# Kernel tuning notes

Measured on AMD Instinct MI355X. Metric: run time of the kernel, lower is better.

The kernel has to match this reference:

```python
import jax, jax.numpy as jnp
import numpy as np

D = 1024

def setup_inputs() -> dict:
    key = jax.random.key(0)
    k1, k2, k3, k4, k5 = jax.random.split(key, 5)
    B, S = 128, 512
    seq_output = jax.random.normal(k1, (B, S, D), dtype=jnp.float32)
    mask = jax.random.randint(k2, (B, S), 0, 2) == 1  # True = masked position
    # ensure last position is never fully-masked pathological: fine either way
    scale1 = 1.0 / np.sqrt(D)
    W1 = jax.random.normal(k3, (D, D), dtype=jnp.float32) * scale1
    b1 = jnp.zeros((D,), dtype=jnp.float32)
    w2 = jax.random.normal(k4, (D,), dtype=jnp.float32) * scale1
    return {"seq_output": seq_output, "mask": mask, "W1": W1, "b1": b1, "w2": w2}

def reference(seq_output, mask, W1, b1, w2):
    # u_last: last timestep embedding
    u_last = seq_output[:, -1, :]                           # [B, D]
    # additive attention MLP: Linear -> tanh -> Linear(D->1, no bias)
    h = jnp.tanh(jnp.einsum('bsd,de->bse', seq_output, W1) + b1)  # [B, S, D]
    scores = jnp.einsum('bsd,d->bs', h, w2)                 # [B, S]
    scores = jnp.where(mask, -1e9, scores)
    attn = jax.nn.softmax(scores, axis=-1)                  # [B, S]
    u_att = jnp.einsum('bs,bsd->bd', attn, seq_output)      # [B, D]
    return (u_last, u_att)
```

## Files before the change

### kernel.cpp

```cpp
#include <hip/hip_runtime.h>
#include <hip/hip_bf16.h>
#include <cstdint>
#include <cstddef>

#define BATCH 128
#define SEQ   512
#define DIM   1024
#define MROWS (BATCH * SEQ)
#define NT    32

typedef short short8 __attribute__((ext_vector_type(8)));
typedef __bf16 bf16x8 __attribute__((ext_vector_type(8)));
typedef float f32x4 __attribute__((ext_vector_type(4)));

template <typename VA> struct other_frag { using type = bf16x8; };
template <> struct other_frag<bf16x8> { using type = short8; };

template <typename VA>
__device__ __forceinline__ auto try_mfma(VA a, VA b, f32x4 c, int)
    -> decltype(__builtin_amdgcn_mfma_f32_16x16x32_bf16(a, b, c, 0, 0, 0)) {
  return __builtin_amdgcn_mfma_f32_16x16x32_bf16(a, b, c, 0, 0, 0);
}
template <typename VA>
__device__ __forceinline__ f32x4 try_mfma(VA a, VA b, f32x4 c, long) {
  using O = typename other_frag<VA>::type;
  O a2 = __builtin_bit_cast(O, a);
  O b2 = __builtin_bit_cast(O, b);
  return __builtin_amdgcn_mfma_f32_16x16x32_bf16(a2, b2, c, 0, 0, 0);
}
__device__ __forceinline__ f32x4 mfma_bf16(short8 a, short8 b, f32x4 c) {
  return try_mfma(a, b, c, 0);
}

__device__ __forceinline__ unsigned short f32_to_bf16(float f) {
  union { float f; uint32_t u; } v; v.f = f;
  uint32_t u = v.u;
  u += 0x7FFFu + ((u >> 16) & 1u);
  return (unsigned short)(u >> 16);
}

__device__ __forceinline__ short8 cvt8(f32x4 a, f32x4 b) {
  bf16x8 o;
  o[0] = (__bf16)a[0]; o[1] = (__bf16)a[1]; o[2] = (__bf16)a[2]; o[3] = (__bf16)a[3];
  o[4] = (__bf16)b[0]; o[5] = (__bf16)b[1]; o[6] = (__bf16)b[2]; o[7] = (__bf16)b[3];
  return __builtin_bit_cast(short8, o);
}

__device__ __forceinline__ void gload_lds16(const void* g, void* l) {
  __builtin_amdgcn_global_load_lds(
      (__attribute__((address_space(1))) void*)g,
      (__attribute__((address_space(3))) void*)l,
      16, 0, 0);
}

__device__ __forceinline__ float fast_tanh(float x) {
  x = fminf(fmaxf(x, -15.0f), 15.0f);
  float e = __expf(2.0f * x);
  return (e - 1.0f) / (e + 1.0f);
}

__global__ __launch_bounds__(256) void w1t_kernel(const float* __restrict__ W1,
                                                  unsigned short* __restrict__ W1t) {
  __shared__ float tile[64][65];
  int bx = blockIdx.x & 15;
  int by = blockIdx.x >> 4;
  int t = threadIdx.x;
  int c = t & 63, r0 = t >> 6;
#pragma unroll
  for (int i = 0; i < 16; i++) {
    int r = i * 4 + r0;
    tile[r][c] = W1[(size_t)(by * 64 + r) * DIM + bx * 64 + c];
  }
  __syncthreads();
#pragma unroll
  for (int i = 0; i < 16; i++) {
    int r = i * 4 + r0;
    W1t[(size_t)(bx * 64 + r) * DIM + by * 64 + c] = f32_to_bf16(tile[c][r]);
  }
}

__global__ __launch_bounds__(512, 2) void gemm_score_kernel(
    const float* __restrict__ X,
    const unsigned short* __restrict__ W1t,
    const float* __restrict__ b1,
    const float* __restrict__ w2,
    float* __restrict__ scores) {
  __shared__ __align__(16) char lds[147456];

  const int tid = threadIdx.x;
  const int lane = tid & 63;
  const int w = tid >> 6;
  const int wr = w >> 1, wc = w & 1;

  const int bx = blockIdx.x;
  const int swz = (bx & 7) * 128 + (bx >> 3);
  const int m0 = (swz >> 2) * 256;
  const int n0 = (swz & 3) * 256;

  const float* aSrc[4];
#pragma unroll
  for (int i = 0; i < 4; i++) {
    int sc = i * 512 + tid;
    int row = sc >> 3;
    int q = (sc & 7) ^ (row & 7) ^ ((row >> 3) & 7);
    aSrc[i] = X + (size_t)(m0 + row) * DIM + q * 4;
  }
  const unsigned short* bSrc[2];
#pragma unroll
  for (int i = 0; i < 2; i++) {
    int sc = i * 512 + tid;
    int srow = sc >> 3;
    int j = (sc & 7) ^ (srow & 7);
    int row = srow * 2 + (j >> 2);
    bSrc[i] = W1t + (size_t)(n0 + row) * DIM + (j & 3) * 8;
  }

  int aOff[4][2];
#pragma unroll
  for (int mi = 0; mi < 4; mi++) {
    int row = wr * 64 + mi * 16 + (lane & 15);
    int m = (row & 7) ^ ((row >> 3) & 7);
#pragma unroll
    for (int c = 0; c < 2; c++) {
      int js = ((lane >> 4) * 2 + c) ^ m;
      aOff[mi][c] = row * 128 + js * 16;
    }
  }
  int bOff[8];
#pragma unroll
  for (int ni = 0; ni < 8; ni++) {
    int row = wc * 128 + ni * 16 + (lane & 15);
    int srow = row >> 1;
    int ic = ((row & 1) * 4 + (lane >> 4)) ^ (srow & 7);
    bOff[ni] = srow * 128 + ic * 16;
  }

  f32x4 acc[4][8];
#pragma unroll
  for (int mi = 0; mi < 4; mi++)
#pragma unroll
    for (int ni = 0; ni < 8; ni++)
      acc[mi][ni] = (f32x4){0.f, 0.f, 0.f, 0.f};

  short8 af[4], bfv[8];

#define STAGE(S) do {                                                   \
    const int bufA_ = ((S) % 3) * 32768;                                \
    const int bufB_ = 98304 + ((S) % 3) * 16384;                        \
    const int koF_ = (S) * 32;                                          \
    gload_lds16(aSrc[0] + koF_, lds + bufA_ + w * 1024);                \
    gload_lds16(aSrc[1] + koF_, lds + bufA_ + 8192 + w * 1024);         \
    gload_lds16(aSrc[2] + koF_, lds + bufA_ + 16384 + w * 1024);        \
    gload_lds16(aSrc[3] + koF_, lds + bufA_ + 24576 + w * 1024);        \
    gload_lds16(bSrc[0] + koF_, lds + bufB_ + w * 1024);                \
    gload_lds16(bSrc[1] + koF_, lds + bufB_ + 8192 + w * 1024);         \
  } while (0)

#define KITER(S, VMSTR) do {                                            \
    asm volatile("s_waitcnt vmcnt(" VMSTR ")" ::: "memory");            \
    __builtin_amdgcn_s_barrier();                                       \
    __builtin_amdgcn_sched_barrier(0);                                  \
    if ((S) + 2 < NT) STAGE((S) + 2);                                   \
    const char* bufA_ = lds + ((S) % 3) * 32768;                        \
    const char* bufB_ = lds + 98304 + ((S) % 3) * 16384;                \
    _Pragma("unroll")                                                   \
    for (int mi = 0; mi < 4; mi++) {                                    \
      f32x4 lo_ = *(const f32x4*)(bufA_ + aOff[mi][0]);                 \
      f32x4 hi_ = *(const f32x4*)(bufA_ + aOff[mi][1]);                 \
      af[mi] = cvt8(lo_, hi_);                                          \
    }                                                                   \
    _Pragma("unroll")                                                   \
    for (int ni = 0; ni < 8; ni++)                                      \
      bfv[ni] = *(const short8*)(bufB_ + bOff[ni]);                     \
    __builtin_amdgcn_s_setprio(1);                                      \
    _Pragma("unroll")                                                   \
    for (int mi = 0; mi < 4; mi++)                                      \
      _Pragma("unroll")                                                 \
      for (int ni = 0; ni < 8; ni++)                                    \
        acc[mi][ni] = mfma_bf16(af[mi], bfv[ni], acc[mi][ni]);          \
    __builtin_amdgcn_s_setprio(0);                                      \
  } while (0)

  STAGE(0); STAGE(1);

  for (int s = 0; s < NT - 1; ++s) KITER(s, "6");
  KITER(NT - 1, "0");

#undef STAGE
#undef KITER

  const int cg = lane >> 4;
  const int cl = lane & 15;
#pragma unroll
  for (int mi = 0; mi < 4; mi++) {
    float p0 = 0.f, p1 = 0.f, p2 = 0.f, p3 = 0.f;
#pragma unroll
    for (int ni = 0; ni < 8; ni++) {
      int col = n0 + wc * 128 + ni * 16 + cl;
      float w2v = w2[col];
      float b1v = b1[col];
      p0 += fast_tanh(acc[mi][ni][0] + b1v) * w2v;
      p1 += fast_tanh(acc[mi][ni][1] + b1v) * w2v;
      p2 += fast_tanh(acc[mi][ni][2] + b1v) * w2v;
      p3 += fast_tanh(acc[mi][ni][3] + b1v) * w2v;
    }
#pragma unroll
    for (int off = 1; off < 16; off <<= 1) {
      p0 += __shfl_xor(p0, off);
      p1 += __shfl_xor(p1, off);
      p2 += __shfl_xor(p2, off);
      p3 += __shfl_xor(p3, off);
    }
    if (cl == 0) {
      int row = m0 + wr * 64 + mi * 16 + cg * 4;
      atomicAdd(&scores[row + 0], p0);
      atomicAdd(&scores[row + 1], p1);
      atomicAdd(&scores[row + 2], p2);
      atomicAdd(&scores[row + 3], p3);
    }
  }
}

__global__ __launch_bounds__(256) void attn_uatt_kernel(
    const float* __restrict__ X,
    const float* __restrict__ scores,
    const int* __restrict__ mask,
    float* __restrict__ u_att,
    float* __restrict__ u_last) {
  const int b = blockIdx.x;
  const int half = blockIdx.y;
  const int tid = threadIdx.x;
  const int lane = tid & 63;
  const int wave = tid >> 6;

  __shared__ float attn[SEQ];
  __shared__ float rbuf[4];
  __shared__ float part[3][64 * 9];

  float s0 = scores[(size_t)b * SEQ + tid];
  float s1 = scores[(size_t)b * SEQ + 256 + tid];
  if (mask[(size_t)b * SEQ + tid]) s0 = -1000000000.0f;
  if (mask[(size_t)b * SEQ + 256 + tid]) s1 = -1000000000.0f;

  float mx = fmaxf(s0, s1);
#pragma unroll
  for (int off = 1; off < 64; off <<= 1) mx = fmaxf(mx, __shfl_xor(mx, off));
  if (lane == 0) rbuf[wave] = mx;
  __syncthreads();
  mx = fmaxf(fmaxf(rbuf[0], rbuf[1]), fmaxf(rbuf[2], rbuf[3]));

  float p0 = expf(s0 - mx), p1 = expf(s1 - mx);
  float sm = p0 + p1;
#pragma unroll
  for (int off = 1; off < 64; off <<= 1) sm += __shfl_xor(sm, off);
  __syncthreads();
  if (lane == 0) rbuf[wave] = sm;
  __syncthreads();
  sm = rbuf[0] + rbuf[1] + rbuf[2] + rbuf[3];
  float inv = 1.0f / sm;
  attn[tid] = p0 * inv;
  attn[tid + 256] = p1 * inv;
  __syncthreads();

  if (tid < 128) {
    ((f32x4*)u_last)[(size_t)b * 256 + half * 128 + tid] =
        ((const f32x4*)X)[((size_t)b * SEQ + (SEQ - 1)) * 256 + half * 128 + tid];
  }

  const int col = tid & 63;
  const int sh = tid >> 6;
  const f32x4* Xp = (const f32x4*)X + (size_t)b * SEQ * 256 + half * 128 + col * 2;
  f32x4 a0 = {0.f, 0.f, 0.f, 0.f}, a1 = {0.f, 0.f, 0.f, 0.f};
  for (int s = sh * 128; s < sh * 128 + 128; s++) {
    float wgt = attn[s];
    a0 += wgt * Xp[(size_t)s * 256];
    a1 += wgt * Xp[(size_t)s * 256 + 1];
  }
  if (sh) {
#pragma unroll
    for (int j = 0; j < 4; j++) part[sh - 1][col * 9 + j] = a0[j];
#pragma unroll
    for (int j = 0; j < 4; j++) part[sh - 1][col * 9 + 4 + j] = a1[j];
  }
  __syncthreads();
  if (sh == 0) {
#pragma unroll
    for (int j = 0; j < 4; j++)
      a0[j] += part[0][col * 9 + j] + part[1][col * 9 + j] + part[2][col * 9 + j];
#pragma unroll
    for (int j = 0; j < 4; j++)
      a1[j] += part[0][col * 9 + 4 + j] + part[1][col * 9 + 4 + j] + part[2][col * 9 + 4 + j];
    f32x4* dst = (f32x4*)(u_att + (size_t)b * DIM + half * 512 + col * 8);
    dst[0] = a0;
    dst[1] = a1;
  }
}

extern "C" void kernel_launch(void* const* d_in, const int* in_sizes, int n_in,
                              void* d_out, int out_size, void* d_ws, size_t ws_size,
                              hipStream_t stream) {
  const float* X    = (const float*)d_in[0];
  const int*   mask = (const int*)d_in[1];
  const float* W1   = (const float*)d_in[2];
  const float* b1   = (const float*)d_in[3];
  const float* w2   = (const float*)d_in[4];

  float* out    = (float*)d_out;
  float* u_last = out;
  float* u_att  = out + BATCH * DIM;

  char* ws = (char*)d_ws;
  unsigned short* W1t = (unsigned short*)ws;
  float* scores = (float*)(ws + (size_t)DIM * DIM * 2);

  hipMemsetAsync(scores, 0, MROWS * sizeof(float), stream);
  hipLaunchKernelGGL(w1t_kernel, dim3(256), dim3(256), 0, stream, W1, W1t);
  hipLaunchKernelGGL(gemm_score_kernel, dim3(1024), dim3(512), 0, stream,
                     X, W1t, b1, w2, scores);
  hipLaunchKernelGGL(attn_uatt_kernel, dim3(128, 2), dim3(256), 0, stream,
                     X, scores, mask, u_att, u_last);
}
```

Before: 226.8 us.

## Convert A tile to bf16 in registers before LDS write, shrinking LDS footprint

Instead of DMA-copying fp32 X tiles directly into LDS and converting to bf16 on every fragment read, each thread loads its fp32 A chunk into registers several iterations ahead, converts it to bf16 once and writes it to a swizzled bf16 LDS buffer. This halves the A buffer size (LDS drops from 144KB to 96KB) and halves LDS read traffic for A, and it may allow more occupancy. In exchange it adds register pressure from three in-flight register sets and a more complex software pipeline with explicit waitcnt bookkeeping, which risks stalls or hazards.

After: 227.1 us. No clear change (+0.1%).

```diff
diff --git a/kernel.cpp b/kernel.cpp
--- a/kernel.cpp
+++ b/kernel.cpp
@@ -85,7 +85,7 @@
     const float* __restrict__ b1,
     const float* __restrict__ w2,
     float* __restrict__ scores) {
-  __shared__ __align__(16) char lds[147456];
+  __shared__ __align__(16) char lds[98304];
 
   const int tid = threadIdx.x;
   const int lane = tid & 63;
@@ -97,14 +97,16 @@
   const int m0 = (swz >> 2) * 256;
   const int n0 = (swz & 3) * 256;
 
-  const float* aSrc[4];
-#pragma unroll
-  for (int i = 0; i < 4; i++) {
-    int sc = i * 512 + tid;
-    int row = sc >> 3;
-    int q = (sc & 7) ^ (row & 7) ^ ((row >> 3) & 7);
-    aSrc[i] = X + (size_t)(m0 + row) * DIM + q * 4;
-  }
+  const float* aSrcT = X + (size_t)(m0 + (tid >> 1)) * DIM + (tid & 1) * 16;
+  int wOff[2];
+  {
+    int srow = tid >> 2;
+    int j0 = ((tid >> 1) & 1) * 4 + (tid & 1) * 2;
+#pragma unroll
+    for (int i = 0; i < 2; i++)
+      wOff[i] = srow * 128 + ((j0 + i) ^ (srow & 7)) * 16;
+  }
+
   const unsigned short* bSrc[2];
 #pragma unroll
   for (int i = 0; i < 2; i++) {
@@ -115,16 +117,13 @@
     bSrc[i] = W1t + (size_t)(n0 + row) * DIM + (j & 3) * 8;
   }
 
-  int aOff[4][2];
+  int aOff[4];
 #pragma unroll
   for (int mi = 0; mi < 4; mi++) {
     int row = wr * 64 + mi * 16 + (lane & 15);
-    int m = (row & 7) ^ ((row >> 3) & 7);
-#pragma unroll
-    for (int c = 0; c < 2; c++) {
-      int js = ((lane >> 4) * 2 + c) ^ m;
-      aOff[mi][c] = row * 128 + js * 16;
-    }
+    int srow = row >> 1;
+    int ic = ((row & 1) * 4 + (lane >> 4)) ^ (srow & 7);
+    aOff[mi] = srow * 128 + ic * 16;
   }
   int bOff[8];
 #pragma unroll
@@ -142,33 +141,43 @@
     for (int ni = 0; ni < 8; ni++)
       acc[mi][ni] = (f32x4){0.f, 0.f, 0.f, 0.f};
 
+  f32x4 sA0[4], sA1[4], sA2[4];
   short8 af[4], bfv[8];
 
-#define STAGE(S) do {                                                   \
-    const int bufA_ = ((S) % 3) * 32768;                                \
-    const int bufB_ = 98304 + ((S) % 3) * 16384;                        \
+#define LOAD_AS(SET, S) do {                                            \
+    const float* p_ = aSrcT + (S) * 32;                                 \
+    SET[0] = *(const f32x4*)(p_);                                       \
+    SET[1] = *(const f32x4*)(p_ + 4);                                   \
+    SET[2] = *(const f32x4*)(p_ + 8);                                   \
+    SET[3] = *(const f32x4*)(p_ + 12);                                  \
+  } while (0)
+
+#define WRITE_A(SET, SLOT) do {                                         \
+    char* aw_ = lds + (SLOT) * 16384;                                   \
+    *(short8*)(aw_ + wOff[0]) = cvt8(SET[0], SET[1]);                   \
+    *(short8*)(aw_ + wOff[1]) = cvt8(SET[2], SET[3]);                   \
+  } while (0)
+
+#define STAGE_B(S, SLOT) do {                                           \
+    char* bb_ = lds + 49152 + (SLOT) * 16384;                           \
     const int koF_ = (S) * 32;                                          \
-    gload_lds16(aSrc[0] + koF_, lds + bufA_ + w * 1024);                \
-    gload_lds16(aSrc[1] + koF_, lds + bufA_ + 8192 + w * 1024);         \
-    gload_lds16(aSrc[2] + koF_, lds + bufA_ + 16384 + w * 1024);        \
-    gload_lds16(aSrc[3] + koF_, lds + bufA_ + 24576 + w * 1024);        \
-    gload_lds16(bSrc[0] + koF_, lds + bufB_ + w * 1024);                \
-    gload_lds16(bSrc[1] + koF_, lds + bufB_ + 8192 + w * 1024);         \
+    gload_lds16(bSrc[0] + koF_, bb_ + w * 1024);                        \
+    gload_lds16(bSrc[1] + koF_, bb_ + 8192 + w * 1024);                 \
   } while (0)
 
-#define KITER(S, VMSTR) do {                                            \
+#define KITER(S, SETW, SETL, RS, WS, BS, W_, PFA, PFB, VMSTR) do {      \
     asm volatile("s_waitcnt vmcnt(" VMSTR ")" ::: "memory");            \
     __builtin_amdgcn_s_barrier();                                       \
     __builtin_amdgcn_sched_barrier(0);                                  \
-    if ((S) + 2 < NT) STAGE((S) + 2);                                   \
-    const char* bufA_ = lds + ((S) % 3) * 32768;                        \
-    const char* bufB_ = lds + 98304 + ((S) % 3) * 16384;                \
+    if (W_) WRITE_A(SETW, WS);                                          \
+    __builtin_amdgcn_sched_barrier(0);                                  \
+    if (PFA) LOAD_AS(SETL, (S) + 3);                                    \
+    if (PFB) STAGE_B((S) + 2, BS);                                      \
+    const char* bufA_ = lds + (RS) * 16384;                             \
+    const char* bufB_ = lds + 49152 + (RS) * 16384;                     \
     _Pragma("unroll")                                                   \
-    for (int mi = 0; mi < 4; mi++) {                                    \
-      f32x4 lo_ = *(const f32x4*)(bufA_ + aOff[mi][0]);                 \
-      f32x4 hi_ = *(const f32x4*)(bufA_ + aOff[mi][1]);                 \
-      af[mi] = cvt8(lo_, hi_);                                          \
-    }                                                                   \
+    for (int mi = 0; mi < 4; mi++)                                      \
+      af[mi] = *(const short8*)(bufA_ + aOff[mi]);                      \
     _Pragma("unroll")                                                   \
     for (int ni = 0; ni < 8; ni++)                                      \
       bfv[ni] = *(const short8*)(bufB_ + bOff[ni]);                     \
@@ -181,13 +190,31 @@
     __builtin_amdgcn_s_setprio(0);                                      \
   } while (0)
 
-  STAGE(0); STAGE(1);
-
-  for (int s = 0; s < NT - 1; ++s) KITER(s, "6");
-  KITER(NT - 1, "0");
-
-#undef STAGE
+  LOAD_AS(sA0, 0);
+  asm volatile("s_waitcnt vmcnt(0)" ::: "memory");
+  WRITE_A(sA0, 0);
+  LOAD_AS(sA1, 1);
+  STAGE_B(0, 0);
+  LOAD_AS(sA2, 2);
+  STAGE_B(1, 1);
+  asm volatile("s_waitcnt lgkmcnt(0)" ::: "memory");
+
+  for (int t = 0; t < 9; ++t) {
+    const int S0 = 3 * t;
+    KITER(S0,     sA1, sA0, 0, 1, 2, 1, 1, 1, "6");
+    KITER(S0 + 1, sA2, sA1, 1, 2, 0, 1, 1, 1, "6");
+    KITER(S0 + 2, sA0, sA2, 2, 0, 1, 1, 1, 1, "6");
+  }
+  KITER(27, sA1, sA0, 0, 1, 2, 1, 1, 1, "6");
+  KITER(28, sA2, sA1, 1, 2, 0, 1, 1, 1, "6");
+  KITER(29, sA0, sA0, 2, 0, 1, 1, 0, 1, "6");
+  KITER(30, sA1, sA0, 0, 1, 2, 1, 0, 0, "2");
+  KITER(31, sA0, sA0, 1, 0, 0, 0, 0, 0, "0");
+
 #undef KITER
+#undef STAGE_B
+#undef WRITE_A
+#undef LOAD_AS
 
   const int cg = lane >> 4;
   const int cl = lane & 15;
```
